# Kernel optimization log

Hardware: AMD Instinct MI355X
Metric: run time of the kernel (lower is better)

## Reference

```python
import jax, jax.numpy as jnp
import numpy as np

D_MODEL = 256; N_HEADS = 8; N_LEVELS = 4; N_POINTS = 4; D_FFN = 1024
BS = 8; NQ = 100; NKPT = 17
LEVEL_SHAPES = [(160, 160), (80, 80), (40, 40), (20, 20)]  # (H, W) per level
LEN_V = sum(h * w for h, w in LEVEL_SHAPES)  # 34000


def layer_norm(x, g, b, eps=1e-5):
    m = x.mean(-1, keepdims=True)
    v = ((x - m) ** 2).mean(-1, keepdims=True)
    return (x - m) * jax.lax.rsqrt(v + eps) * g + b


def mha(q, k, v, Wqkv, bqkv, Wo, bo):
    # torch nn.MultiheadAttention, batch_first, eval mode (no dropout)
    d = q.shape[-1]; dh = d // N_HEADS
    def proj(x, W, b):
        return (x @ W.T + b).reshape(*x.shape[:-1], N_HEADS, dh)
    qp = proj(q, Wqkv[:d], bqkv[:d])
    kp = proj(k, Wqkv[d:2 * d], bqkv[d:2 * d])
    vp = proj(v, Wqkv[2 * d:], bqkv[2 * d:])
    att = jnp.einsum('bqhd,bkhd->bhqk', qp, kp) / jnp.sqrt(jnp.asarray(dh, q.dtype))
    att = jax.nn.softmax(att, -1)
    out = jnp.einsum('bhqk,bkhd->bqhd', att, vp).reshape(q.shape)
    return out @ Wo.T + bo


def bilinear_sample(val, loc, h, w):
    # val: (B, H, h*w, Dh); loc: (B, Lq, H, P, 2) normalized to [0,1]
    # matches F.grid_sample(align_corners=False, padding_mode='zeros') on grid 2*loc-1
    B, Lq, H, P, _ = loc.shape
    px = loc[..., 0] * w - 0.5
    py = loc[..., 1] * h - 0.5
    x0f = jnp.floor(px); y0f = jnp.floor(py)
    lx = px - x0f; ly = py - y0f
    x0 = x0f.astype(jnp.int32); y0 = y0f.astype(jnp.int32)
    out = jnp.zeros((B, H, Lq, P, val.shape[-1]), val.dtype)
    for dx, dy, wt in ((0, 0, (1 - lx) * (1 - ly)), (1, 0, lx * (1 - ly)),
                       (0, 1, (1 - lx) * ly), (1, 1, lx * ly)):
        xi = x0 + dx; yi = y0 + dy
        valid = ((xi >= 0) & (xi < w) & (yi >= 0) & (yi < h)).astype(val.dtype)
        idx = jnp.clip(yi, 0, h - 1) * w + jnp.clip(xi, 0, w - 1)  # (B,Lq,H,P)
        idx = idx.transpose(0, 2, 1, 3).reshape(B, H, Lq * P)
        g = jnp.take_along_axis(val, idx[..., None], axis=2).reshape(B, H, Lq, P, -1)
        out = out + g * (wt * valid).transpose(0, 2, 1, 3)[..., None]
    return out  # (B, H, Lq, P, Dh)


def ms_deform_attn(query, ref_points, memory, off_W, off_b, aw_W, aw_b,
                   val_W, val_b, outp_W, outp_b):
    B, Lq, _ = query.shape
    dh = D_MODEL // N_HEADS
    value = (memory @ val_W.T + val_b).reshape(B, LEN_V, N_HEADS, dh)
    off = (query @ off_W.T + off_b).reshape(B, Lq, N_HEADS, N_LEVELS, N_POINTS, 2)
    aw = (query @ aw_W.T + aw_b).reshape(B, Lq, N_HEADS, N_LEVELS * N_POINTS)
    aw = jax.nn.softmax(aw, -1).reshape(B, Lq, N_HEADS, N_LEVELS, N_POINTS)
    normalizer = jnp.array([[w, h] for h, w in LEVEL_SHAPES], dtype=query.dtype)  # (L,2) as (W,H)
    loc = ref_points[:, :, None, :, None, :] + off / normalizer[None, None, None, :, None, :]
    out = jnp.zeros((B, Lq, N_HEADS, dh), query.dtype)
    start = 0
    for l, (h, w) in enumerate(LEVEL_SHAPES):
        vl = value[:, start:start + h * w].transpose(0, 2, 1, 3)  # (B,H,hw,Dh)
        s = bilinear_sample(vl, loc[:, :, :, l], h, w)            # (B,H,Lq,P,Dh)
        out = out + jnp.einsum('bhqpd,bqhp->bqhd', s, aw[:, :, :, l])
        start += h * w
    return out.reshape(B, Lq, D_MODEL) @ outp_W.T + outp_b


def setup_inputs() -> dict:
    key = jax.random.key(0)
    ks = iter(jax.random.split(key, 40))
    d = D_MODEL
    def w(shape, s=0.02):
        return jax.random.normal(next(ks), shape, jnp.float32) * s
    inp = {
        'tgt_pose': jax.random.normal(next(ks), (BS, NQ, NKPT, d), jnp.float32),
        'tgt_pose_query_pos': jax.random.normal(next(ks), (BS, NQ, NKPT, d), jnp.float32),
        'tgt_pose_reference_points': jax.random.uniform(next(ks), (BS, NQ * NKPT, N_LEVELS, 2), jnp.float32),
        'memory': jax.random.normal(next(ks), (BS, LEN_V, d), jnp.float32),
        'win_Wqkv': w((3 * d, d)), 'win_bqkv': jnp.zeros((3 * d,), jnp.float32),
        'win_Wo': w((d, d)), 'win_bo': jnp.zeros((d,), jnp.float32),
        'win_ng': jnp.ones((d,), jnp.float32), 'win_nb': jnp.zeros((d,), jnp.float32),
        'acr_Wqkv': w((3 * d, d)), 'acr_bqkv': jnp.zeros((3 * d,), jnp.float32),
        'acr_Wo': w((d, d)), 'acr_bo': jnp.zeros((d,), jnp.float32),
        'acr_ng': jnp.ones((d,), jnp.float32), 'acr_nb': jnp.zeros((d,), jnp.float32),
        'off_W': w((N_HEADS * N_LEVELS * N_POINTS * 2, d)),
        'off_b': jax.random.uniform(next(ks), (N_HEADS * N_LEVELS * N_POINTS * 2,), jnp.float32, -1.0, 1.0),
        'aw_W': w((N_HEADS * N_LEVELS * N_POINTS, d)), 'aw_b': jnp.zeros((N_HEADS * N_LEVELS * N_POINTS,), jnp.float32),
        'val_W': w((d, d)), 'val_b': jnp.zeros((d,), jnp.float32),
        'outp_W': w((d, d)), 'outp_b': jnp.zeros((d,), jnp.float32),
        'gate_W': w((2 * d, 2 * d)), 'gate_b': jnp.zeros((2 * d,), jnp.float32),
        'gate_ng': jnp.ones((d,), jnp.float32), 'gate_nb': jnp.zeros((d,), jnp.float32),
        'ffn_W1': w((D_FFN, d)), 'ffn_b1': jnp.zeros((D_FFN,), jnp.float32),
        'ffn_W2': w((d, D_FFN)), 'ffn_b2': jnp.zeros((d,), jnp.float32),
        'n2_g': jnp.ones((d,), jnp.float32), 'n2_b': jnp.zeros((d,), jnp.float32),
        'memory_spatial_shapes': jnp.array(LEVEL_SHAPES, jnp.int32),
    }
    return inp


def reference(tgt_pose, tgt_pose_query_pos, tgt_pose_reference_points, memory,
              win_Wqkv, win_bqkv, win_Wo, win_bo, win_ng, win_nb,
              acr_Wqkv, acr_bqkv, acr_Wo, acr_bo, acr_ng, acr_nb,
              off_W, off_b, aw_W, aw_b, val_W, val_b, outp_W, outp_b,
              gate_W, gate_b, gate_ng, gate_nb,
              ffn_W1, ffn_b1, ffn_W2, ffn_b2, n2_g, n2_b,
              memory_spatial_shapes):
    bs, nq, K, d = tgt_pose.shape
    # with_pos_embed mutates tgt_pose in place in the torch code -> residual includes pos
    tgt = tgt_pose + tgt_pose_query_pos
    # within-attention over keypoints of each query
    x = tgt.reshape(bs * nq, K, d)
    t2 = mha(x, x, x, win_Wqkv, win_bqkv, win_Wo, win_bo).reshape(bs, nq, K, d)
    tgt = layer_norm(tgt + t2, win_ng, win_nb)
    # across-attention over queries for each keypoint
    xk = tgt.transpose(0, 2, 1, 3).reshape(bs * K, nq, d)
    t2 = mha(xk, xk, xk, acr_Wqkv, acr_bqkv, acr_Wo, acr_bo)
    tgt = layer_norm(xk + t2, acr_ng, acr_nb).reshape(bs, K, nq, d).transpose(0, 2, 1, 3)
    # second in-place pos add before deformable cross-attn (also feeds gateway)
    tgt_q = tgt + tgt_pose_query_pos
    t2 = ms_deform_attn(tgt_q.reshape(bs, nq * K, d), tgt_pose_reference_points, memory,
                        off_W, off_b, aw_W, aw_b, val_W, val_b, outp_W, outp_b)
    t2 = t2.reshape(bs, nq, K, d)
    # Gate
    g = jax.nn.sigmoid(jnp.concatenate([tgt_q, t2], -1) @ gate_W.T + gate_b)
    g1, g2 = jnp.split(g, 2, -1)
    tgt = layer_norm(g1 * tgt_q + g2 * t2, gate_ng, gate_nb)
    # FFN
    h = jax.nn.relu(tgt @ ffn_W1.T + ffn_b1)
    tgt = tgt + h @ ffn_W2.T + ffn_b2
    tgt = layer_norm(jnp.clip(tgt, -65504.0, 65504.0), n2_g, n2_b)
    return tgt
```

## Files before the change

kernel.cpp:

```cpp
#include <hip/hip_runtime.h>
#include <hip/hip_bf16.h>

#define NH 8
#define BS_ 8
#define NQ_ 100
#define NK_ 17
#define LQ 1700
#define T_TOK 13600
#define LEN_VV 34000

typedef __attribute__((ext_vector_type(8))) short short8v;
typedef __attribute__((ext_vector_type(8))) __bf16 bf16x8;
typedef __attribute__((ext_vector_type(4))) float f32x4;

__device__ __forceinline__ short f2bf(float f){
  __hip_bfloat16 h = __float2bfloat16(f);
  return *reinterpret_cast<short*>(&h);
}
__device__ __forceinline__ float bf2f(short s){
  return __uint_as_float(((uint)(unsigned short)s) << 16);
}

template<int EPI, int ADDA, int SWZ, int INB>
__global__ __launch_bounds__(256) void mgemm_k(const void* __restrict__ Av,
                                               const float* __restrict__ A2,
                                               const float* __restrict__ W,
                                               const float* __restrict__ bias,
                                               __hip_bfloat16* __restrict__ Cb,
                                               int M, int N, int K, int nbx){
  __shared__ short sh[128 * 136];
  short* As = sh;
  short* Ws = sh + 128 * 64;
  int j;
  if (SWZ){
    int total = gridDim.x;
    int q = total >> 3, r = total & 7;
    int x = blockIdx.x & 7, k = blockIdx.x >> 3;
    j = (x < r) ? x * (q + 1) + k : r * (q + 1) + (x - r) * q + k;
  } else {
    j = blockIdx.x;
  }
  const float* A = (const float*)Av;
  const short* Ab = (const short*)Av;
  const int tid = threadIdx.x;
  const int bm = (j / nbx) * 128, bn = (j % nbx) * 128;
  const int wave = tid >> 6, lane = tid & 63;
  const int wm = (wave >> 1) * 64, wn = (wave & 1) * 64;
  const int s = tid & 7;
  const int row0 = tid >> 3;
  f32x4 acc[4][4] = {};
  const int lrow = lane & 15, lk = lane >> 4;

  float4 ra[INB ? 1 : 8], rw[8];
  short8v rab[INB ? 4 : 1];
#pragma unroll
  for (int i = 0; i < 4; i++){
    int row = row0 + i * 32;
    int gr = bm + row;
    if (INB){
      short8v z = {};
      rab[INB ? i : 0] = (gr < M) ? *(const short8v*)(Ab + (size_t)gr * K + s * 8) : z;
    } else {
      float4 z = make_float4(0.f, 0.f, 0.f, 0.f);
      if (gr < M){
        const float* p = A + (size_t)gr * K + s * 8;
        float4 x0 = ((const float4*)p)[0], x1 = ((const float4*)p)[1];
        if (ADDA){
          const float* q2 = A2 + (size_t)gr * K + s * 8;
          float4 y0 = ((const float4*)q2)[0], y1 = ((const float4*)q2)[1];
          x0.x+=y0.x; x0.y+=y0.y; x0.z+=y0.z; x0.w+=y0.w;
          x1.x+=y1.x; x1.y+=y1.y; x1.z+=y1.z; x1.w+=y1.w;
        }
        ra[INB ? 0 : (2 * i)] = x0; ra[INB ? 0 : (2 * i + 1)] = x1;
      } else { ra[INB ? 0 : (2 * i)] = z; ra[INB ? 0 : (2 * i + 1)] = z; }
    }
    const float* q = W + (size_t)(bn + row) * K + s * 8;
    rw[2 * i] = ((const float4*)q)[0]; rw[2 * i + 1] = ((const float4*)q)[1];
  }

  for (int k0 = 0; k0 < K; k0 += 64){
#pragma unroll
    for (int i = 0; i < 4; i++){
      int row = row0 + i * 32;
      int sw = ((s ^ (row & 7)) << 3) + row * 64;
      if (INB){
        *(short8v*)&As[sw] = rab[INB ? i : 0];
      } else {
        float4 a0 = ra[INB ? 0 : (2 * i)], a1 = ra[INB ? 0 : (2 * i + 1)];
        short8v v;
        v[0]=f2bf(a0.x); v[1]=f2bf(a0.y); v[2]=f2bf(a0.z); v[3]=f2bf(a0.w);
        v[4]=f2bf(a1.x); v[5]=f2bf(a1.y); v[6]=f2bf(a1.z); v[7]=f2bf(a1.w);
        *(short8v*)&As[sw] = v;
      }
      float4 a0 = rw[2 * i], a1 = rw[2 * i + 1];
      short8v u;
      u[0]=f2bf(a0.x); u[1]=f2bf(a0.y); u[2]=f2bf(a0.z); u[3]=f2bf(a0.w);
      u[4]=f2bf(a1.x); u[5]=f2bf(a1.y); u[6]=f2bf(a1.z); u[7]=f2bf(a1.w);
      *(short8v*)&Ws[sw] = u;
    }
    __syncthreads();
    if (k0 + 64 < K){
#pragma unroll
      for (int i = 0; i < 4; i++){
        int row = row0 + i * 32;
        int gr = bm + row;
        if (INB){
          short8v z = {};
          rab[INB ? i : 0] = (gr < M) ? *(const short8v*)(Ab + (size_t)gr * K + k0 + 64 + s * 8) : z;
        } else {
          float4 z = make_float4(0.f, 0.f, 0.f, 0.f);
          if (gr < M){
            const float* p = A + (size_t)gr * K + k0 + 64 + s * 8;
            float4 x0 = ((const float4*)p)[0], x1 = ((const float4*)p)[1];
            if (ADDA){
              const float* q2 = A2 + (size_t)gr * K + k0 + 64 + s * 8;
              float4 y0 = ((const float4*)q2)[0], y1 = ((const float4*)q2)[1];
              x0.x+=y0.x; x0.y+=y0.y; x0.z+=y0.z; x0.w+=y0.w;
              x1.x+=y1.x; x1.y+=y1.y; x1.z+=y1.z; x1.w+=y1.w;
            }
            ra[INB ? 0 : (2 * i)] = x0; ra[INB ? 0 : (2 * i + 1)] = x1;
          } else { ra[INB ? 0 : (2 * i)] = z; ra[INB ? 0 : (2 * i + 1)] = z; }
        }
        const float* q = W + (size_t)(bn + row) * K + k0 + 64 + s * 8;
        rw[2 * i] = ((const float4*)q)[0]; rw[2 * i + 1] = ((const float4*)q)[1];
      }
    }
#pragma unroll
    for (int ks = 0; ks < 2; ks++){
      short8v af[4], bw[4];
      int slot = ks * 4 + lk;
#pragma unroll
      for (int m = 0; m < 4; m++){
        int r = wm + m * 16 + lrow;
        af[m] = *(const short8v*)&As[r * 64 + ((slot ^ (r & 7)) << 3)];
      }
#pragma unroll
      for (int n = 0; n < 4; n++){
        int r = wn + n * 16 + lrow;
        bw[n] = *(const short8v*)&Ws[r * 64 + ((slot ^ (r & 7)) << 3)];
      }
#pragma unroll
      for (int m = 0; m < 4; m++)
#pragma unroll
        for (int n = 0; n < 4; n++)
          acc[m][n] = __builtin_amdgcn_mfma_f32_16x16x32_bf16(
              __builtin_bit_cast(bf16x8, af[m]),
              __builtin_bit_cast(bf16x8, bw[n]), acc[m][n], 0, 0, 0);
    }
    __syncthreads();
  }
  const int STR = 136;
// ... 12 lines not shown
      }
    }
  }
  __syncthreads();
#pragma unroll
  for (int it = 0; it < 8; it++){
    int r = it * 16 + (tid >> 4);
    int chunk = tid & 15;
    if (bm + r < M){
      uint4 v = *(const uint4*)((const char*)sh + r * 272 + chunk * 16);
      *(uint4*)((char*)Cb + ((size_t)(bm + r) * N + bn) * 2 + chunk * 16) = v;
    }
  }
}

template<int EPI, int OUTB, int INB, int DUALA>
__global__ __launch_bounds__(256) void g64_k(const void* __restrict__ Av,
                                             const void* __restrict__ A1v,
                                             const float* __restrict__ W0,
                                             const float* __restrict__ W1,
                                             int NSPLIT,
                                             const float* __restrict__ bias0,
                                             const float* __restrict__ bias1,
                                             const float* __restrict__ RES,
                                             float* __restrict__ Cf,
                                             __hip_bfloat16* __restrict__ Cb,
                                             int M, int N, int K, int sA){
  __shared__ short sh64[2 * 64 * 64];
  short* As = sh64;
  short* Ws = sh64 + 64 * 64;
  const int tid = threadIdx.x;
  const int bn = blockIdx.x * 64, bm = blockIdx.y * 64;
  const int wave = tid >> 6, lane = tid & 63;
  const int wm = (wave >> 1) * 32, wn = (wave & 1) * 32;
  const int s = tid & 7, row0 = tid >> 3;
  const int lrow = lane & 15, lk = lane >> 4;
  f32x4 acc[2][2] = {};

  for (int k0 = 0; k0 < K; k0 += 64){
#pragma unroll
    for (int i = 0; i < 2; i++){
      int row = row0 + i * 32;
      int sw = ((s ^ (row & 7)) << 3) + row * 64;
      short8v v = {};
      int gr = bm + row;
      if (gr < M){
        if (INB){
          v = *(const short8v*)((const short*)Av + (size_t)gr * sA + k0 + s * 8);
        } else {
          const float* Ap;
          if (DUALA) Ap = (k0 < 256) ? (const float*)Av + (size_t)gr * 256 + k0
                                     : (const float*)A1v + (size_t)gr * 256 + (k0 - 256);
          else Ap = (const float*)Av + (size_t)gr * sA + k0;
          float4 a0 = ((const float4*)(Ap + s * 8))[0];
          float4 a1 = ((const float4*)(Ap + s * 8))[1];
          v[0]=f2bf(a0.x); v[1]=f2bf(a0.y); v[2]=f2bf(a0.z); v[3]=f2bf(a0.w);
          v[4]=f2bf(a1.x); v[5]=f2bf(a1.y); v[6]=f2bf(a1.z); v[7]=f2bf(a1.w);
        }
      }
      *(short8v*)&As[sw] = v;
      int wr = bn + row;
      const float* Wp = (wr < NSPLIT) ? W0 + (size_t)wr * K + k0
                                      : W1 + (size_t)(wr - NSPLIT) * K + k0;
      float4 b0 = ((const float4*)(Wp + s * 8))[0];
      float4 b1 = ((const float4*)(Wp + s * 8))[1];
      short8v u;
      u[0]=f2bf(b0.x); u[1]=f2bf(b0.y); u[2]=f2bf(b0.z); u[3]=f2bf(b0.w);
      u[4]=f2bf(b1.x); u[5]=f2bf(b1.y); u[6]=f2bf(b1.z); u[7]=f2bf(b1.w);
      *(short8v*)&Ws[sw] = u;
    }
    __syncthreads();
#pragma unroll
    for (int ks = 0; ks < 2; ks++){
      int slot = ks * 4 + lk;
      short8v af[2], bw[2];
#pragma unroll
      for (int m = 0; m < 2; m++){
        int r = wm + m * 16 + lrow;
        af[m] = *(const short8v*)&As[r * 64 + ((slot ^ (r & 7)) << 3)];
      }
#pragma unroll
      for (int n = 0; n < 2; n++){
        int r = wn + n * 16 + lrow;
        bw[n] = *(const short8v*)&Ws[r * 64 + ((slot ^ (r & 7)) << 3)];
      }
#pragma unroll
      for (int m = 0; m < 2; m++)
#pragma unroll
        for (int n = 0; n < 2; n++)
          acc[m][n] = __builtin_amdgcn_mfma_f32_16x16x32_bf16(
              __builtin_bit_cast(bf16x8, af[m]),
              __builtin_bit_cast(bf16x8, bw[n]), acc[m][n], 0, 0, 0);
    }
    __syncthreads();
  }
  if (OUTB){
    const int STR = 72;
#pragma unroll
    for (int n = 0; n < 2; n++){
      int col = wn + n * 16 + lrow;
      int gc = bn + col;
      float bsv = (gc < NSPLIT) ? bias0[gc] : bias1[gc - NSPLIT];
#pragma unroll
      for (int m = 0; m < 2; m++){
#pragma unroll
        for (int i = 0; i < 4; i++){
          int row = wm + m * 16 + lk * 4 + i;
          float c = acc[m][n][i] + bsv;
          if (EPI == 1) c = fmaxf(c, 0.f);
          if (EPI == 2) c = 1.f / (1.f + expf(-c));
          sh64[row * STR + col] = f2bf(c);
        }
      }
    }
    __syncthreads();
#pragma unroll
    for (int it = 0; it < 2; it++){
      int r = it * 32 + (tid >> 3);
      int chunk = tid & 7;
      if (bm + r < M){
        uint4 v = *(const uint4*)((const char*)sh64 + r * 144 + chunk * 16);
        *(uint4*)((char*)Cb + ((size_t)(bm + r) * N + bn) * 2 + chunk * 16) = v;
      }
    }
  } else {
#pragma unroll
    for (int n = 0; n < 2; n++){
      int gc = bn + wn + n * 16 + lrow;
      float bsv = (gc < NSPLIT) ? bias0[gc] : bias1[gc - NSPLIT];
#pragma unroll
      for (int m = 0; m < 2; m++){
#pragma unroll
        for (int i = 0; i < 4; i++){
          int row = bm + wm + m * 16 + lk * 4 + i;
          if (row >= M) continue;
          float c = acc[m][n][i] + bsv;
          if (EPI == 1) c = fmaxf(c, 0.f);
          if (EPI == 2) c = 1.f / (1.f + expf(-c));
          if (EPI == 3) c += RES[(size_t)row * N + gc];
          Cf[(size_t)row * N + gc] = c;
        }
      }
    }
  }
}

template<int SITE, int OUTB>
__global__ __launch_bounds__(512) void gln_k(const short* __restrict__ Abf,
                                             const float* __restrict__ W,
                                             const float* __restrict__ bias,
                                             const float* __restrict__ r0,
                                             const float* __restrict__ r1,
                                             const float* __restrict__ g,
                                             const float* __restrict__ be,
                                             void* __restrict__ outv,
                                             int M, int K){
  __shared__ short As[64 * 64];
  __shared__ short Ws[256 * 64];
  __shared__ float part[64][4][2];
  __shared__ float stats[64][2];
  const int tid = threadIdx.x;
  const int bm = blockIdx.x * 64;
  const int wave = tid >> 6, lane = tid & 63;
  const int wm = (wave >> 2) * 32, wn = (wave & 3) * 64;
  const int s = tid & 7, row0 = tid >> 3;
  const int lrow = lane & 15, lk = lane >> 4;
  f32x4 acc[2][4] = {};

  short8v pa = {};
  { int gr = bm + row0; if (gr < M) pa = *(const short8v*)(Abf + (size_t)gr * K + s * 8); }
  float4 pw[8];
#pragma unroll
  for (int i = 0; i < 4; i++){
    const float* wp = W + (size_t)(row0 + i * 64) * K + s * 8;
    pw[2 * i] = ((const float4*)wp)[0]; pw[2 * i + 1] = ((const float4*)wp)[1];
  }

  for (int k0 = 0; k0 < K; k0 += 64){
    *(short8v*)&As[row0 * 64 + ((s ^ (row0 & 7)) << 3)] = pa;
#pragma unroll
    for (int i = 0; i < 4; i++){
      int row = row0 + i * 64;
      float4 b0 = pw[2 * i], b1 = pw[2 * i + 1];
      short8v u;
      u[0]=f2bf(b0.x); u[1]=f2bf(b0.y); u[2]=f2bf(b0.z); u[3]=f2bf(b0.w);
      u[4]=f2bf(b1.x); u[5]=f2bf(b1.y); u[6]=f2bf(b1.z); u[7]=f2bf(b1.w);
      *(short8v*)&Ws[row * 64 + ((s ^ (row & 7)) << 3)] = u;
    }
    __syncthreads();
    if (k0 + 64 < K){
      int gr = bm + row0;
      pa = (short8v){};
      if (gr < M) pa = *(const short8v*)(Abf + (size_t)gr * K + k0 + 64 + s * 8);
#pragma unroll
      for (int i = 0; i < 4; i++){
        const float* wp = W + (size_t)(row0 + i * 64) * K + k0 + 64 + s * 8;
        pw[2 * i] = ((const float4*)wp)[0]; pw[2 * i + 1] = ((const float4*)wp)[1];
      }
    }
#pragma unroll
    for (int ks = 0; ks < 2; ks++){
      int slot = ks * 4 + lk;
      short8v af[2], bw[4];
#pragma unroll
      for (int m = 0; m < 2; m++){
        int r = wm + m * 16 + lrow;
        af[m] = *(const short8v*)&As[r * 64 + ((slot ^ (r & 7)) << 3)];
      }
#pragma unroll
      for (int n = 0; n < 4; n++){
        int r = wn + n * 16 + lrow;
        bw[n] = *(const short8v*)&Ws[r * 64 + ((slot ^ (r & 7)) << 3)];
      }
#pragma unroll
      for (int m = 0; m < 2; m++)
#pragma unroll
        for (int n = 0; n < 4; n++)
          acc[m][n] = __builtin_amdgcn_mfma_f32_16x16x32_bf16(
              __builtin_bit_cast(bf16x8, af[m]),
              __builtin_bit_cast(bf16x8, bw[n]), acc[m][n], 0, 0, 0);
    }
    __syncthreads();
  }

#pragma unroll
  for (int m = 0; m < 2; m++){
#pragma unroll
    for (int i = 0; i < 4; i++){
      int row = wm + m * 16 + lk * 4 + i;
      int grow = bm + row;
      float s1 = 0.f, s2 = 0.f;
      if (grow < M){
#pragma unroll
        for (int n = 0; n < 4; n++){
          int col = wn + n * 16 + lrow;
          float x = acc[m][n][i] + bias[col] + r0[(size_t)grow * 256 + col];
          if (SITE == 0) x += r1[(size_t)grow * 256 + col];
          if (SITE == 2) x = fminf(fmaxf(x, -65504.f), 65504.f);
          acc[m][n][i] = x;
          s1 += x; s2 += x * x;
        }
      }
#pragma unroll
      for (int msk = 1; msk <= 8; msk <<= 1){
        s1 += __shfl_xor(s1, msk, 64);
        s2 += __shfl_xor(s2, msk, 64);
      }
      if (lrow == 0){ part[row][wave & 3][0] = s1; part[row][wave & 3][1] = s2; }
    }
  }
  __syncthreads();
  if (tid < 64){
    float s1 = part[tid][0][0] + part[tid][1][0] + part[tid][2][0] + part[tid][3][0];
    float s2 = part[tid][0][1] + part[tid][1][1] + part[tid][2][1] + part[tid][3][1];
    float mean = s1 * (1.f / 256.f);
    float var = s2 * (1.f / 256.f) - mean * mean;
    stats[tid][0] = mean;
    stats[tid][1] = rsqrtf(fmaxf(var, 0.f) + 1e-5f);
  }
  __syncthreads();
#pragma unroll
  for (int m = 0; m < 2; m++){
#pragma unroll
    for (int i = 0; i < 4; i++){
      int row = wm + m * 16 + lk * 4 + i;
      int grow = bm + row;
      if (grow >= M) continue;
      float mean = stats[row][0], rstd = stats[row][1];
      size_t orow = grow;
      if (SITE == 0){
        int bi = grow / LQ; int rem = grow % LQ; int q = rem / NK_; int kk = rem % NK_;
        orow = (size_t)bi * LQ + kk * NQ_ + q;
      }
#pragma unroll
      for (int n = 0; n < 4; n++){
        int col = wn + n * 16 + lrow;
        float o = (acc[m][n][i] - mean) * rstd * g[col] + be[col];
        if (OUTB) ((short*)outv)[orow * 256 + col] = f2bf(o);
        else      ((float*)outv)[orow * 256 + col] = o;
      }
    }
  }
}

__global__ __launch_bounds__(512) void glnoa_k(const short* __restrict__ Abf,
                                               const float* __restrict__ W,
                                               const float* __restrict__ bias,
                                               const short* __restrict__ r0b,
                                               const float* __restrict__ qpos,
                                               const float* __restrict__ g,
                                               const float* __restrict__ be,
                                               short* __restrict__ TQout,
                                               float* __restrict__ OFFAW,
                                               const float* __restrict__ off_W,
                                               const float* __restrict__ aw_W,
                                               const float* __restrict__ off_b,
                                               const float* __restrict__ aw_b,
                                               int M){
  __shared__ short smem[64 * 256 + 384 * 64];
  short* As1 = smem;
  short* Ws1 = smem + 64 * 64;
  float* part = (float*)(smem + 64 * 64 + 256 * 64);
  float* stats = part + 64 * 4 * 2;
  short* As2 = smem;
  short* Ws2 = smem + 64 * 256;
  const int K = 256;
  const int tid = threadIdx.x;
  const int bm = blockIdx.x * 64;
  const int wave = tid >> 6, lane = tid & 63;
  const int wm = (wave >> 2) * 32, wn = (wave & 3) * 64;
  const int s = tid & 7, row0 = tid >> 3;
  const int lrow = lane & 15, lk = lane >> 4;
  f32x4 acc[2][4] = {};

  short8v pa = {};
  { int gr = bm + row0; if (gr < M) pa = *(const short8v*)(Abf + (size_t)gr * K + s * 8); }
  float4 pw[8];
#pragma unroll
  for (int i = 0; i < 4; i++){
    const float* wp = W + (size_t)(row0 + i * 64) * K + s * 8;
    pw[2 * i] = ((const float4*)wp)[0]; pw[2 * i + 1] = ((const float4*)wp)[1];
  }
  for (int k0 = 0; k0 < K; k0 += 64){
    *(short8v*)&As1[row0 * 64 + ((s ^ (row0 & 7)) << 3)] = pa;
#pragma unroll
    for (int i = 0; i < 4; i++){
      int row = row0 + i * 64;
      float4 b0 = pw[2 * i], b1 = pw[2 * i + 1];
      short8v u;
      u[0]=f2bf(b0.x); u[1]=f2bf(b0.y); u[2]=f2bf(b0.z); u[3]=f2bf(b0.w);
      u[4]=f2bf(b1.x); u[5]=f2bf(b1.y); u[6]=f2bf(b1.z); u[7]=f2bf(b1.w);
      *(short8v*)&Ws1[row * 64 + ((s ^ (row & 7)) << 3)] = u;
    }
    __syncthreads();
    if (k0 + 64 < K){
      int gr = bm + row0;
      pa = (short8v){};
      if (gr < M) pa = *(const short8v*)(Abf + (size_t)gr * K + k0 + 64 + s * 8);
#pragma unroll
      for (int i = 0; i < 4; i++){
        const float* wp = W + (size_t)(row0 + i * 64) * K + k0 + 64 + s * 8;
        pw[2 * i] = ((const float4*)wp)[0]; pw[2 * i + 1] = ((const float4*)wp)[1];
      }
    }
#pragma unroll
    for (int ks = 0; ks < 2; ks++){
      int slot = ks * 4 + lk;
      short8v af[2], bw[4];
#pragma unroll
      for (int m = 0; m < 2; m++){
        int r = wm + m * 16 + lrow;
        af[m] = *(const short8v*)&As1[r * 64 + ((slot ^ (r & 7)) << 3)];
      }
#pragma unroll
      for (int n = 0; n < 4; n++){
        int r = wn + n * 16 + lrow;
        bw[n] = *(const short8v*)&Ws1[r * 64 + ((slot ^ (r & 7)) << 3)];
      }
#pragma unroll
      for (int m = 0; m < 2; m++)
#pragma unroll
        for (int n = 0; n < 4; n++)
          acc[m][n] = __builtin_amdgcn_mfma_f32_16x16x32_bf16(
              __builtin_bit_cast(bf16x8, af[m]),
              __builtin_bit_cast(bf16x8, bw[n]), acc[m][n], 0, 0, 0);
    }
    __syncthreads();
  }
#pragma unroll
  for (int m = 0; m < 2; m++){
#pragma unroll
    for (int i = 0; i < 4; i++){
      int row = wm + m * 16 + lk * 4 + i;
      int grow = bm + row;
      float s1 = 0.f, s2 = 0.f;
      if (grow < M){
#pragma unroll
        for (int n = 0; n < 4; n++){
          int col = wn + n * 16 + lrow;
          float x = acc[m][n][i] + bias[col] + bf2f(r0b[(size_t)grow * 256 + col]);
          acc[m][n][i] = x;
          s1 += x; s2 += x * x;
        }
      }
#pragma unroll
      for (int msk = 1; msk <= 8; msk <<= 1){
        s1 += __shfl_xor(s1, msk, 64);
        s2 += __shfl_xor(s2, msk, 64);
      }
      if (lrow == 0){ part[(row * 4 + (wave & 3)) * 2] = s1; part[(row * 4 + (wave & 3)) * 2 + 1] = s2; }
    }
  }
  __syncthreads();
  if (tid < 64){
    float s1 = part[(tid * 4 + 0) * 2] + part[(tid * 4 + 1) * 2] + part[(tid * 4 + 2) * 2] + part[(tid * 4 + 3) * 2];
    float s2 = part[(tid * 4 + 0) * 2 + 1] + part[(tid * 4 + 1) * 2 + 1] + part[(tid * 4 + 2) * 2 + 1] + part[(tid * 4 + 3) * 2 + 1];
    float mean = s1 * (1.f / 256.f);
    float var = s2 * (1.f / 256.f) - mean * mean;
    stats[tid * 2] = mean;
    stats[tid * 2 + 1] = rsqrtf(fmaxf(var, 0.f) + 1e-5f);
  }
  __syncthreads();
#pragma unroll
  for (int m = 0; m < 2; m++){
#pragma unroll
    for (int i = 0; i < 4; i++){
      int row = wm + m * 16 + lk * 4 + i;
      int grow = bm + row;
      float mean = stats[row * 2], rstd = stats[row * 2 + 1];
      size_t orow = 0;
      if (grow < M){
        int bi = grow / LQ; int rem = grow % LQ; int kk = rem / NQ_; int q = rem % NQ_;
        orow = (size_t)bi * LQ + q * NK_ + kk;
      }
#pragma unroll
      for (int n = 0; n < 4; n++){
        int col = wn + n * 16 + lrow;
        float tq = 0.f;
        if (grow < M){
          float o = (acc[m][n][i] - mean) * rstd * g[col] + be[col];
          tq = o + qpos[orow * 256 + col];
          TQout[orow * 256 + col] = f2bf(tq);
        }
        As2[row * 256 + ((((col >> 3) ^ (row & 7)) << 3) + (col & 7))] = f2bf(tq);
      }
    }
  }
  __syncthreads();
  const int wm2 = (wave >> 2) * 32, wn2 = (wave & 3) * 96;
  f32x4 acc2[2][6] = {};
  for (int k0 = 0; k0 < 256; k0 += 64){
#pragma unroll
    for (int it = 0; it < 6; it++){
      int wr = row0 + it * 64;
      const float* Wp = (wr < 256) ? off_W + (size_t)wr * 256 + k0
                                   : aw_W + (size_t)(wr - 256) * 256 + k0;
      float4 b0 = ((const float4*)(Wp + s * 8))[0];
      float4 b1 = ((const float4*)(Wp + s * 8))[1];
      short8v u;
      u[0]=f2bf(b0.x); u[1]=f2bf(b0.y); u[2]=f2bf(b0.z); u[3]=f2bf(b0.w);
      u[4]=f2bf(b1.x); u[5]=f2bf(b1.y); u[6]=f2bf(b1.z); u[7]=f2bf(b1.w);
      *(short8v*)&Ws2[wr * 64 + ((s ^ (wr & 7)) << 3)] = u;
    }
    __syncthreads();
#pragma unroll
    for (int ks = 0; ks < 2; ks++){
      int slotl = ks * 4 + lk;
      int slotg = (k0 >> 3) + slotl;
      short8v af[2], bw[6];
#pragma unroll
      for (int m = 0; m < 2; m++){
        int r = wm2 + m * 16 + lrow;
        af[m] = *(const short8v*)&As2[r * 256 + ((slotg ^ (r & 7)) << 3)];
      }
#pragma unroll
      for (int n = 0; n < 6; n++){
        int r = wn2 + n * 16 + lrow;
        bw[n] = *(const short8v*)&Ws2[r * 64 + ((slotl ^ (r & 7)) << 3)];
      }
#pragma unroll
      for (int m = 0; m < 2; m++)
#pragma unroll
        for (int n = 0; n < 6; n++)
          acc2[m][n] = __builtin_amdgcn_mfma_f32_16x16x32_bf16(
              __builtin_bit_cast(bf16x8, af[m]),
              __builtin_bit_cast(bf16x8, bw[n]), acc2[m][n], 0, 0, 0);
    }
    __syncthreads();
  }
#pragma unroll
  for (int m = 0; m < 2; m++){
#pragma unroll
    for (int i = 0; i < 4; i++){
      int row = wm2 + m * 16 + lk * 4 + i;
      int grow = bm + row;
      if (grow >= M) continue;
      int bi = grow / LQ; int rem = grow % LQ; int kk = rem / NQ_; int q = rem % NQ_;
      size_t orow = (size_t)bi * LQ + q * NK_ + kk;
#pragma unroll
      for (int n = 0; n < 6; n++){
        int col = wn2 + n * 16 + lrow;
        float c = acc2[m][n][i] + ((col < 256) ? off_b[col] : aw_b[col - 256]);
        OFFAW[orow * 384 + col] = c;
      }
    }
  }
}

__global__ __launch_bounds__(512) void gateln_k(const short* __restrict__ TQ,
                                                const short* __restrict__ T2,
                                                const float* __restrict__ W,
                                                const float* __restrict__ bias,
                                                const float* __restrict__ g,
                                                const float* __restrict__ be,
                                                float* __restrict__ out, int M){
  __shared__ short sh[64 * 64 + 512 * 64];
  short* As = sh;
  short* Ws = sh + 64 * 64;
  const int tid = threadIdx.x;
  const int bm = blockIdx.x * 64;
  const int wave = tid >> 6, lane = tid & 63;
  const int wm = (wave >> 2) * 32, wn = (wave & 3) * 128;
  const int s = tid & 7, row0 = tid >> 3;
  const int lrow = lane & 15, lk = lane >> 4;
  f32x4 acc[2][8] = {};

  for (int k0 = 0; k0 < 512; k0 += 64){
    {
      short8v v = {};
      int gr = bm + row0;
      if (gr < M){
        v = (k0 < 256) ? *(const short8v*)(TQ + (size_t)gr * 256 + k0 + s * 8)
                       : *(const short8v*)(T2 + (size_t)gr * 256 + (k0 - 256) + s * 8);
      }
      *(short8v*)&As[row0 * 64 + ((s ^ (row0 & 7)) << 3)] = v;
    }
#pragma unroll
    for (int i = 0; i < 8; i++){
      int row = row0 + i * 64;
      const float* wp = W + (size_t)row * 512 + k0 + s * 8;
      float4 b0 = ((const float4*)wp)[0], b1 = ((const float4*)wp)[1];
      short8v u;
      u[0]=f2bf(b0.x); u[1]=f2bf(b0.y); u[2]=f2bf(b0.z); u[3]=f2bf(b0.w);
      u[4]=f2bf(b1.x); u[5]=f2bf(b1.y); u[6]=f2bf(b1.z); u[7]=f2bf(b1.w);
      *(short8v*)&Ws[row * 64 + ((s ^ (row & 7)) << 3)] = u;
    }
    __syncthreads();
#pragma unroll
    for (int ks = 0; ks < 2; ks++){
      int slot = ks * 4 + lk;
      short8v af[2], bw[8];
#pragma unroll
      for (int m = 0; m < 2; m++){
        int r = wm + m * 16 + lrow;
        af[m] = *(const short8v*)&As[r * 64 + ((slot ^ (r & 7)) << 3)];
      }
#pragma unroll
      for (int n = 0; n < 8; n++){
        int r = wn + n * 16 + lrow;
        bw[n] = *(const short8v*)&Ws[r * 64 + ((slot ^ (r & 7)) << 3)];
      }
#pragma unroll
      for (int m = 0; m < 2; m++)
#pragma unroll
        for (int n = 0; n < 8; n++)
          acc[m][n] = __builtin_amdgcn_mfma_f32_16x16x32_bf16(
              __builtin_bit_cast(bf16x8, af[m]),
              __builtin_bit_cast(bf16x8, bw[n]), acc[m][n], 0, 0, 0);
    }
    __syncthreads();
  }
  short* gb = sh;
  const int GSTR = 520;
#pragma unroll
  for (int n = 0; n < 8; n++){
    int col = wn + n * 16 + lrow;
    float bsv = bias[col];
#pragma unroll
    for (int m = 0; m < 2; m++){
#pragma unroll
      for (int i = 0; i < 4; i++){
        int row = wm + m * 16 + lk * 4 + i;
        float c = acc[m][n][i] + bsv;
        gb[row * GSTR + col] = f2bf(1.f / (1.f + __expf(-c)));
      }
    }
  }
  __syncthreads();
  {
    int row = tid >> 3, cg = tid & 7;
    int grow = bm + row;
    float x[32];
    float s1 = 0.f, s2 = 0.f;
    if (grow < M){
#pragma unroll
      for (int jv = 0; jv < 4; jv++){
        int c0 = cg * 32 + jv * 8;
        short8v aqv = *(const short8v*)(TQ + (size_t)grow * 256 + c0);
        short8v t2v = *(const short8v*)(T2 + (size_t)grow * 256 + c0);
#pragma unroll
        for (int jj = 0; jj < 8; jj++){
          float g1 = bf2f(gb[row * GSTR + c0 + jj]);
          float g2 = bf2f(gb[row * GSTR + 256 + c0 + jj]);
          float xv = g1 * bf2f(aqv[jj]) + g2 * bf2f(t2v[jj]);
          x[jv * 8 + jj] = xv; s1 += xv; s2 += xv * xv;
        }
      }
    }
    s1 += __shfl_xor(s1, 1, 64); s2 += __shfl_xor(s2, 1, 64);
    s1 += __shfl_xor(s1, 2, 64); s2 += __shfl_xor(s2, 2, 64);
    s1 += __shfl_xor(s1, 4, 64); s2 += __shfl_xor(s2, 4, 64);
    float mean = s1 * (1.f / 256.f);
    float var = s2 * (1.f / 256.f) - mean * mean;
    float rstd = rsqrtf(fmaxf(var, 0.f) + 1e-5f);
    if (grow < M){
#pragma unroll
      for (int jv = 0; jv < 4; jv++){
        int c0 = cg * 32 + jv * 8;
        float4 o0, o1;
#pragma unroll
        for (int jj = 0; jj < 8; jj++){
          int c = c0 + jj;
          float o = (x[jv * 8 + jj] - mean) * rstd * g[c] + be[c];
          if (jj < 4) ((float*)&o0)[jj] = o; else ((float*)&o1)[jj - 4] = o;
        }
        *(float4*)(out + (size_t)grow * 256 + c0) = o0;
        *(float4*)(out + (size_t)grow * 256 + c0 + 4) = o1;
      }
    }
  }
}

template<int TP, int NSPL>
__global__ __launch_bounds__(256) void mha_mfma_k(const short* __restrict__ qkv,
                                                  __hip_bfloat16* __restrict__ out, int S){
// ... 221 lines not shown
                              hipStream_t stream){
  const float* tgt_pose = (const float*)d_in[0];
  const float* qpos     = (const float*)d_in[1];
  const float* refp     = (const float*)d_in[2];
  const float* memory   = (const float*)d_in[3];
  const float* win_Wqkv = (const float*)d_in[4];
  const float* win_bqkv = (const float*)d_in[5];
  const float* win_Wo   = (const float*)d_in[6];
  const float* win_bo   = (const float*)d_in[7];
  const float* win_ng   = (const float*)d_in[8];
  const float* win_nb   = (const float*)d_in[9];
  const float* acr_Wqkv = (const float*)d_in[10];
  const float* acr_bqkv = (const float*)d_in[11];
  const float* acr_Wo   = (const float*)d_in[12];
  const float* acr_bo   = (const float*)d_in[13];
  const float* acr_ng   = (const float*)d_in[14];
  const float* acr_nb   = (const float*)d_in[15];
  const float* off_W    = (const float*)d_in[16];
  const float* off_b    = (const float*)d_in[17];
  const float* aw_W     = (const float*)d_in[18];
  const float* aw_b     = (const float*)d_in[19];
  const float* val_W    = (const float*)d_in[20];
  const float* val_b    = (const float*)d_in[21];
  const float* outp_W   = (const float*)d_in[22];
  const float* outp_b   = (const float*)d_in[23];
  const float* gate_W   = (const float*)d_in[24];
  const float* gate_b   = (const float*)d_in[25];
  const float* gate_ng  = (const float*)d_in[26];
  const float* gate_nb  = (const float*)d_in[27];
  const float* ffn_W1   = (const float*)d_in[28];
  const float* ffn_b1   = (const float*)d_in[29];
  const float* ffn_W2   = (const float*)d_in[30];
  const float* ffn_b2   = (const float*)d_in[31];
  const float* n2_g     = (const float*)d_in[32];
  const float* n2_b     = (const float*)d_in[33];

  float* out = (float*)d_out;
  char* ws = (char*)d_ws;
  const size_t TB = (size_t)T_TOK * 256 * 4;
  float* B2 = (float*)(ws);
  char* p = ws + TB;
  short* B1b = (short*)p;  p += (size_t)T_TOK * 256 * 2;
  short* Qb  = (short*)p;  p += (size_t)T_TOK * 768 * 2;
  short* ABF = (short*)p;  p += (size_t)T_TOK * 256 * 2;
  short* TQb = (short*)p;  p += (size_t)T_TOK * 256 * 2;
  short* T2b = (short*)p;  p += (size_t)T_TOK * 256 * 2;
  float* OFFAW = (float*)p; p += (size_t)T_TOK * 384 * 4;
  char* Vregion = p;
  __hip_bfloat16* V = (__hip_bfloat16*)Vregion;
  short* FF = (short*)Vregion;

  const int GM128 = (T_TOK + 127) / 128;
  const int GM64  = (T_TOK + 63) / 64;
  const int BIG = 1 << 30;

  mgemm_k<0,0,1,0><<<2 * 2125, 256, 0, stream>>>(memory, nullptr, val_W, val_b, V, BS_ * LEN_VV, 256, 256, 2);
  mgemm_k<0,1,0,0><<<6 * GM128, 256, 0, stream>>>(tgt_pose, qpos, win_Wqkv, win_bqkv, (__hip_bfloat16*)Qb, T_TOK, 768, 256, 6);
  mha_mfma_k<32,1><<<800 * 4, 256, 0, stream>>>(Qb, (__hip_bfloat16*)ABF, 17);
  gln_k<0,1><<<GM64, 512, 0, stream>>>(ABF, win_Wo, win_bo, tgt_pose, qpos, win_ng, win_nb, B1b, T_TOK, 256);
  mgemm_k<0,0,0,1><<<6 * GM128, 256, 0, stream>>>(B1b, nullptr, acr_Wqkv, acr_bqkv, (__hip_bfloat16*)Qb, T_TOK, 768, 256, 6);
  mha_mfma_k<112,2><<<136 * 8, 256, 0, stream>>>(Qb, (__hip_bfloat16*)ABF, 100);
  glnoa_k<<<GM64, 512, 0, stream>>>(ABF, acr_Wo, acr_bo, B1b, qpos, acr_ng, acr_nb,
                                    TQb, OFFAW, off_W, aw_W, off_b, aw_b, T_TOK);
  deform_k<<<T_TOK / 4, 256, 0, stream>>>(V, OFFAW, refp, (unsigned int*)ABF);
  g64_k<0,1,1,0><<<dim3(4, GM64), 256, 0, stream>>>(ABF, nullptr, outp_W, outp_W, BIG, outp_b, outp_b, nullptr, nullptr, (__hip_bfloat16*)T2b, T_TOK, 256, 256, 256);
  gateln_k<<<GM64, 512, 0, stream>>>(TQb, T2b, gate_W, gate_b, gate_ng, gate_nb, B2, T_TOK);
  mgemm_k<1,0,0,0><<<8 * GM128, 256, 0, stream>>>(B2, nullptr, ffn_W1, ffn_b1, (__hip_bfloat16*)FF, T_TOK, 1024, 256, 8);
  gln_k<2,0><<<GM64, 512, 0, stream>>>(FF, ffn_W2, ffn_b2, B2, nullptr, n2_g, n2_b, out, T_TOK, 1024);
}
```

Baseline: 463.7 us.

## Shrink fused GEMM+LayerNorm kernels to 32-row tiles with 256 threads

The fused GEMM+LayerNorm kernels (gln_k, glnoa_k, gateln_k) now use 32-row M tiles and 256-thread blocks instead of 64 rows and 512 threads, which doubles the grid size. The weight prefetch registers in gln_k/glnoa_k are converted to bf16 at load time, and a cvt8 helper factors out the fp32-to-bf16 packing. The goal is better CU occupancy and load balance on the fused row-LN kernels, since a full row must be resident per block. The cost is that each block re-stages the whole weight matrix for half as many rows, which doubles the weight traffic per row.

```diff
diff --git a/kernel.cpp b/kernel.cpp
--- a/kernel.cpp
+++ b/kernel.cpp
@@ -19,6 +19,12 @@
 }
 __device__ __forceinline__ float bf2f(short s){
   return __uint_as_float(((uint)(unsigned short)s) << 16);
+}
+__device__ __forceinline__ short8v cvt8(float4 a, float4 b){
+  short8v u;
+  u[0]=f2bf(a.x); u[1]=f2bf(a.y); u[2]=f2bf(a.z); u[3]=f2bf(a.w);
+  u[4]=f2bf(b.x); u[5]=f2bf(b.y); u[6]=f2bf(b.z); u[7]=f2bf(b.w);
+  return u;
 }
 
 template<int EPI, int ADDA, int SWZ, int INB>
@@ -86,17 +92,9 @@
       if (INB){
         *(short8v*)&As[sw] = rab[INB ? i : 0];
       } else {
-        float4 a0 = ra[INB ? 0 : (2 * i)], a1 = ra[INB ? 0 : (2 * i + 1)];
-        short8v v;
-        v[0]=f2bf(a0.x); v[1]=f2bf(a0.y); v[2]=f2bf(a0.z); v[3]=f2bf(a0.w);
-        v[4]=f2bf(a1.x); v[5]=f2bf(a1.y); v[6]=f2bf(a1.z); v[7]=f2bf(a1.w);
-        *(short8v*)&As[sw] = v;
-      }
-      float4 a0 = rw[2 * i], a1 = rw[2 * i + 1];
-      short8v u;
-      u[0]=f2bf(a0.x); u[1]=f2bf(a0.y); u[2]=f2bf(a0.z); u[3]=f2bf(a0.w);
-      u[4]=f2bf(a1.x); u[5]=f2bf(a1.y); u[6]=f2bf(a1.z); u[7]=f2bf(a1.w);
-      *(short8v*)&Ws[sw] = u;
+        *(short8v*)&As[sw] = cvt8(ra[INB ? 0 : (2 * i)], ra[INB ? 0 : (2 * i + 1)]);
+      }
+      *(short8v*)&Ws[sw] = cvt8(rw[2 * i], rw[2 * i + 1]);
     }
     __syncthreads();
     if (k0 + 64 < K){
@@ -215,22 +213,14 @@
           if (DUALA) Ap = (k0 < 256) ? (const float*)Av + (size_t)gr * 256 + k0
                                      : (const float*)A1v + (size_t)gr * 256 + (k0 - 256);
           else Ap = (const float*)Av + (size_t)gr * sA + k0;
-          float4 a0 = ((const float4*)(Ap + s * 8))[0];
-          float4 a1 = ((const float4*)(Ap + s * 8))[1];
-          v[0]=f2bf(a0.x); v[1]=f2bf(a0.y); v[2]=f2bf(a0.z); v[3]=f2bf(a0.w);
-          v[4]=f2bf(a1.x); v[5]=f2bf(a1.y); v[6]=f2bf(a1.z); v[7]=f2bf(a1.w);
+          v = cvt8(((const float4*)(Ap + s * 8))[0], ((const float4*)(Ap + s * 8))[1]);
         }
       }
       *(short8v*)&As[sw] = v;
       int wr = bn + row;
       const float* Wp = (wr < NSPLIT) ? W0 + (size_t)wr * K + k0
                                       : W1 + (size_t)(wr - NSPLIT) * K + k0;
-      float4 b0 = ((const float4*)(Wp + s * 8))[0];
-      float4 b1 = ((const float4*)(Wp + s * 8))[1];
-      short8v u;
-      u[0]=f2bf(b0.x); u[1]=f2bf(b0.y); u[2]=f2bf(b0.z); u[3]=f2bf(b0.w);
-      u[4]=f2bf(b1.x); u[5]=f2bf(b1.y); u[6]=f2bf(b1.z); u[7]=f2bf(b1.w);
-      *(short8v*)&Ws[sw] = u;
+      *(short8v*)&Ws[sw] = cvt8(((const float4*)(Wp + s * 8))[0], ((const float4*)(Wp + s * 8))[1]);
     }
     __syncthreads();
 #pragma unroll
@@ -309,7 +299,7 @@
 }
 
 template<int SITE, int OUTB>
-__global__ __launch_bounds__(512) void gln_k(const short* __restrict__ Abf,
+__global__ __launch_bounds__(256) void gln_k(const short* __restrict__ Abf,
                                              const float* __restrict__ W,
                                              const float* __restrict__ bias,
                                              const float* __restrict__ r0,
@@ -318,37 +308,33 @@
                                              const float* __restrict__ be,
                                              void* __restrict__ outv,
                                              int M, int K){
-  __shared__ short As[64 * 64];
+  __shared__ short As[32 * 64];
   __shared__ short Ws[256 * 64];
-  __shared__ float part[64][4][2];
-  __shared__ float stats[64][2];
+  __shared__ float part[32][4][2];
+  __shared__ float stats[32][2];
   const int tid = threadIdx.x;
-  const int bm = blockIdx.x * 64;
+  const int bm = blockIdx.x * 32;
   const int wave = tid >> 6, lane = tid & 63;
-  const int wm = (wave >> 2) * 32, wn = (wave & 3) * 64;
+  const int wn = wave * 64;
   const int s = tid & 7, row0 = tid >> 3;
   const int lrow = lane & 15, lk = lane >> 4;
   f32x4 acc[2][4] = {};
 
   short8v pa = {};
   { int gr = bm + row0; if (gr < M) pa = *(const short8v*)(Abf + (size_t)gr * K + s * 8); }
-  float4 pw[8];
-#pragma unroll
-  for (int i = 0; i < 4; i++){
-    const float* wp = W + (size_t)(row0 + i * 64) * K + s * 8;
-    pw[2 * i] = ((const float4*)wp)[0]; pw[2 * i + 1] = ((const float4*)wp)[1];
+  short8v pwb[8];
+#pragma unroll
+  for (int i = 0; i < 8; i++){
+    const float* wp = W + (size_t)(row0 + i * 32) * K + s * 8;
+    pwb[i] = cvt8(((const float4*)wp)[0], ((const float4*)wp)[1]);
   }
 
   for (int k0 = 0; k0 < K; k0 += 64){
     *(short8v*)&As[row0 * 64 + ((s ^ (row0 & 7)) << 3)] = pa;
 #pragma unroll
-    for (int i = 0; i < 4; i++){
-      int row = row0 + i * 64;
-      float4 b0 = pw[2 * i], b1 = pw[2 * i + 1];
-      short8v u;
-      u[0]=f2bf(b0.x); u[1]=f2bf(b0.y); u[2]=f2bf(b0.z); u[3]=f2bf(b0.w);
-      u[4]=f2bf(b1.x); u[5]=f2bf(b1.y); u[6]=f2bf(b1.z); u[7]=f2bf(b1.w);
-      *(short8v*)&Ws[row * 64 + ((s ^ (row & 7)) << 3)] = u;
+    for (int i = 0; i < 8; i++){
+      int row = row0 + i * 32;
+      *(short8v*)&Ws[row * 64 + ((s ^ (row & 7)) << 3)] = pwb[i];
     }
     __syncthreads();
     if (k0 + 64 < K){
@@ -356,9 +342,9 @@
       pa = (short8v){};
       if (gr < M) pa = *(const short8v*)(Abf + (size_t)gr * K + k0 + 64 + s * 8);
 #pragma unroll
-      for (int i = 0; i < 4; i++){
-        const float* wp = W + (size_t)(row0 + i * 64) * K + k0 + 64 + s * 8;
-        pw[2 * i] = ((const float4*)wp)[0]; pw[2 * i + 1] = ((const float4*)wp)[1];
+      for (int i = 0; i < 8; i++){
+        const float* wp = W + (size_t)(row0 + i * 32) * K + k0 + 64 + s * 8;
+        pwb[i] = cvt8(((const float4*)wp)[0], ((const float4*)wp)[1]);
       }
     }
 #pragma unroll
@@ -367,7 +353,7 @@
       short8v af[2], bw[4];
 #pragma unroll
       for (int m = 0; m < 2; m++){
-        int r = wm + m * 16 + lrow;
+        int r = m * 16 + lrow;
         af[m] = *(const short8v*)&As[r * 64 + ((slot ^ (r & 7)) << 3)];
       }
 #pragma unroll
@@ -390,7 +376,7 @@
   for (int m = 0; m < 2; m++){
 #pragma unroll
     for (int i = 0; i < 4; i++){
-      int row = wm + m * 16 + lk * 4 + i;
+      int row = m * 16 + lk * 4 + i;
       int grow = bm + row;
       float s1 = 0.f, s2 = 0.f;
       if (grow < M){
@@ -409,11 +395,11 @@
         s1 += __shfl_xor(s1, msk, 64);
         s2 += __shfl_xor(s2, msk, 64);
       }
-      if (lrow == 0){ part[row][wave & 3][0] = s1; part[row][wave & 3][1] = s2; }
+      if (lrow == 0){ part[row][wave][0] = s1; part[row][wave][1] = s2; }
     }
   }
   __syncthreads();
-  if (tid < 64){
+  if (tid < 32){
     float s1 = part[tid][0][0] + part[tid][1][0] + part[tid][2][0] + part[tid][3][0];
     float s2 = part[tid][0][1] + part[tid][1][1] + part[tid][2][1] + part[tid][3][1];
     float mean = s1 * (1.f / 256.f);
@@ -426,7 +412,7 @@
   for (int m = 0; m < 2; m++){
 #pragma unroll
     for (int i = 0; i < 4; i++){
-      int row = wm + m * 16 + lk * 4 + i;
+      int row = m * 16 + lk * 4 + i;
       int grow = bm + row;
       if (grow >= M) continue;
       float mean = stats[row][0], rstd = stats[row][1];
@@ -446,7 +432,7 @@
   }
 }
 
-__global__ __launch_bounds__(512) void glnoa_k(const short* __restrict__ Abf,
+__global__ __launch_bounds__(256) void glnoa_k(const short* __restrict__ Abf,
                                                const float* __restrict__ W,
                                                const float* __restrict__ bias,
                                                const short* __restrict__ r0b,
@@ -460,40 +446,36 @@
                                                const float* __restrict__ off_b,
                                                const float* __restrict__ aw_b,
                                                int M){
-  __shared__ short smem[64 * 256 + 384 * 64];
+  __shared__ short smem[32 * 256 + 384 * 64];
+  __shared__ float part[32][4][2];
+  __shared__ float stats[32][2];
   short* As1 = smem;
-  short* Ws1 = smem + 64 * 64;
-  float* part = (float*)(smem + 64 * 64 + 256 * 64);
-  float* stats = part + 64 * 4 * 2;
+  short* Ws1 = smem + 32 * 64;
   short* As2 = smem;
-  short* Ws2 = smem + 64 * 256;
+  short* Ws2 = smem + 32 * 256;
   const int K = 256;
   const int tid = threadIdx.x;
-  const int bm = blockIdx.x * 64;
+  const int bm = blockIdx.x * 32;
   const int wave = tid >> 6, lane = tid & 63;
-  const int wm = (wave >> 2) * 32, wn = (wave & 3) * 64;
+  const int wn = wave * 64;
   const int s = tid & 7, row0 = tid >> 3;
   const int lrow = lane & 15, lk = lane >> 4;
   f32x4 acc[2][4] = {};
 
   short8v pa = {};
   { int gr = bm + row0; if (gr < M) pa = *(const short8v*)(Abf + (size_t)gr * K + s * 8); }
-  float4 pw[8];
-#pragma unroll
-  for (int i = 0; i < 4; i++){
-    const float* wp = W + (size_t)(row0 + i * 64) * K + s * 8;
-    pw[2 * i] = ((const float4*)wp)[0]; pw[2 * i + 1] = ((const float4*)wp)[1];
+  short8v pwb[8];
+#pragma unroll
+  for (int i = 0; i < 8; i++){
+    const float* wp = W + (size_t)(row0 + i * 32) * K + s * 8;
+    pwb[i] = cvt8(((const float4*)wp)[0], ((const float4*)wp)[1]);
   }
   for (int k0 = 0; k0 < K; k0 += 64){
     *(short8v*)&As1[row0 * 64 + ((s ^ (row0 & 7)) << 3)] = pa;
 #pragma unroll
-    for (int i = 0; i < 4; i++){
-      int row = row0 + i * 64;
-      float4 b0 = pw[2 * i], b1 = pw[2 * i + 1];
-      short8v u;
-      u[0]=f2bf(b0.x); u[1]=f2bf(b0.y); u[2]=f2bf(b0.z); u[3]=f2bf(b0.w);
-      u[4]=f2bf(b1.x); u[5]=f2bf(b1.y); u[6]=f2bf(b1.z); u[7]=f2bf(b1.w);
-      *(short8v*)&Ws1[row * 64 + ((s ^ (row & 7)) << 3)] = u;
+    for (int i = 0; i < 8; i++){
+      int row = row0 + i * 32;
+      *(short8v*)&Ws1[row * 64 + ((s ^ (row & 7)) << 3)] = pwb[i];
     }
     __syncthreads();
     if (k0 + 64 < K){
@@ -501,9 +483,9 @@
       pa = (short8v){};
       if (gr < M) pa = *(const short8v*)(Abf + (size_t)gr * K + k0 + 64 + s * 8);
 #pragma unroll
-      for (int i = 0; i < 4; i++){
-        const float* wp = W + (size_t)(row0 + i * 64) * K + k0 + 64 + s * 8;
-        pw[2 * i] = ((const float4*)wp)[0]; pw[2 * i + 1] = ((const float4*)wp)[1];
+      for (int i = 0; i < 8; i++){
+        const float* wp = W + (size_t)(row0 + i * 32) * K + k0 + 64 + s * 8;
+        pwb[i] = cvt8(((const float4*)wp)[0], ((const float4*)wp)[1]);
       }
     }
 #pragma unroll
@@ -512,7 +494,7 @@
       short8v af[2], bw[4];
 #pragma unroll
       for (int m = 0; m < 2; m++){
-        int r = wm + m * 16 + lrow;
+        int r = m * 16 + lrow;
         af[m] = *(const short8v*)&As1[r * 64 + ((slot ^ (r & 7)) << 3)];
       }
 #pragma unroll
@@ -534,7 +516,7 @@
   for (int m = 0; m < 2; m++){
 #pragma unroll
     for (int i = 0; i < 4; i++){
-      int row = wm + m * 16 + lk * 4 + i;
+      int row = m * 16 + lk * 4 + i;
       int grow = bm + row;
       float s1 = 0.f, s2 = 0.f;
       if (grow < M){
@@ -551,26 +533,26 @@
         s1 += __shfl_xor(s1, msk, 64);
         s2 += __shfl_xor(s2, msk, 64);
       }
-      if (lrow == 0){ part[(row * 4 + (wave & 3)) * 2] = s1; part[(row * 4 + (wave & 3)) * 2 + 1] = s2; }
+      if (lrow == 0){ part[row][wave][0] = s1; part[row][wave][1] = s2; }
     }
   }
   __syncthreads();
-  if (tid < 64){
-    float s1 = part[(tid * 4 + 0) * 2] + part[(tid * 4 + 1) * 2] + part[(tid * 4 + 2) * 2] + part[(tid * 4 + 3) * 2];
-    float s2 = part[(tid * 4 + 0) * 2 + 1] + part[(tid * 4 + 1) * 2 + 1] + part[(tid * 4 + 2) * 2 + 1] + part[(tid * 4 + 3) * 2 + 1];
+  if (tid < 32){
+    float s1 = part[tid][0][0] + part[tid][1][0] + part[tid][2][0] + part[tid][3][0];
+    float s2 = part[tid][0][1] + part[tid][1][1] + part[tid][2][1] + part[tid][3][1];
     float mean = s1 * (1.f / 256.f);
     float var = s2 * (1.f / 256.f) - mean * mean;
-    stats[tid * 2] = mean;
-    stats[tid * 2 + 1] = rsqrtf(fmaxf(var, 0.f) + 1e-5f);
+    stats[tid][0] = mean;
+    stats[tid][1] = rsqrtf(fmaxf(var, 0.f) + 1e-5f);
   }
   __syncthreads();
 #pragma unroll
   for (int m = 0; m < 2; m++){
 #pragma unroll
     for (int i = 0; i < 4; i++){
-      int row = wm + m * 16 + lk * 4 + i;
+      int row = m * 16 + lk * 4 + i;
       int grow = bm + row;
-      float mean = stats[row * 2], rstd = stats[row * 2 + 1];
+      float mean = stats[row][0], rstd = stats[row][1];
       size_t orow = 0;
       if (grow < M){
         int bi = grow / LQ; int rem = grow % LQ; int kk = rem / NQ_; int q = rem % NQ_;
@@ -590,20 +572,16 @@
     }
   }
   __syncthreads();
-  const int wm2 = (wave >> 2) * 32, wn2 = (wave & 3) * 96;
+  const int wn2 = wave * 96;
   f32x4 acc2[2][6] = {};
   for (int k0 = 0; k0 < 256; k0 += 64){
 #pragma unroll
-    for (int it = 0; it < 6; it++){
-      int wr = row0 + it * 64;
+    for (int it = 0; it < 12; it++){
+      int wr = row0 + it * 32;
       const float* Wp = (wr < 256) ? off_W + (size_t)wr * 256 + k0
                                    : aw_W + (size_t)(wr - 256) * 256 + k0;
-      float4 b0 = ((const float4*)(Wp + s * 8))[0];
-      float4 b1 = ((const float4*)(Wp + s * 8))[1];
-      short8v u;
-      u[0]=f2bf(b0.x); u[1]=f2bf(b0.y); u[2]=f2bf(b0.z); u[3]=f2bf(b0.w);
-      u[4]=f2bf(b1.x); u[5]=f2bf(b1.y); u[6]=f2bf(b1.z); u[7]=f2bf(b1.w);
-      *(short8v*)&Ws2[wr * 64 + ((s ^ (wr & 7)) << 3)] = u;
+      *(short8v*)&Ws2[wr * 64 + ((s ^ (wr & 7)) << 3)] =
+          cvt8(((const float4*)(Wp + s * 8))[0], ((const float4*)(Wp + s * 8))[1]);
     }
     __syncthreads();
 #pragma unroll
@@ -613,7 +591,7 @@
       short8v af[2], bw[6];
 #pragma unroll
       for (int m = 0; m < 2; m++){
-        int r = wm2 + m * 16 + lrow;
+        int r = m * 16 + lrow;
         af[m] = *(const short8v*)&As2[r * 256 + ((slotg ^ (r & 7)) << 3)];
       }
 #pragma unroll
@@ -635,7 +613,7 @@
   for (int m = 0; m < 2; m++){
 #pragma unroll
     for (int i = 0; i < 4; i++){
-      int row = wm2 + m * 16 + lk * 4 + i;
+      int row = m * 16 + lk * 4 + i;
       int grow = bm + row;
       if (grow >= M) continue;
       int bi = grow / LQ; int rem = grow % LQ; int kk = rem / NQ_; int q = rem % NQ_;
@@ -650,20 +628,20 @@
   }
 }
 
-__global__ __launch_bounds__(512) void gateln_k(const short* __restrict__ TQ,
+__global__ __launch_bounds__(256) void gateln_k(const short* __restrict__ TQ,
                                                 const short* __restrict__ T2,
                                                 const float* __restrict__ W,
                                                 const float* __restrict__ bias,
                                                 const float* __restrict__ g,
                                                 const float* __restrict__ be,
                                                 float* __restrict__ out, int M){
-  __shared__ short sh[64 * 64 + 512 * 64];
+  __shared__ short sh[32 * 64 + 512 * 64];
   short* As = sh;
-  short* Ws = sh + 64 * 64;
+  short* Ws = sh + 32 * 64;
   const int tid = threadIdx.x;
-  const int bm = blockIdx.x * 64;
+  const int bm = blockIdx.x * 32;
   const int wave = tid >> 6, lane = tid & 63;
-  const int wm = (wave >> 2) * 32, wn = (wave & 3) * 128;
+  const int wn = wave * 128;
   const int s = tid & 7, row0 = tid >> 3;
   const int lrow = lane & 15, lk = lane >> 4;
   f32x4 acc[2][8] = {};
@@ -679,14 +657,11 @@
       *(short8v*)&As[row0 * 64 + ((s ^ (row0 & 7)) << 3)] = v;
     }
 #pragma unroll
-    for (int i = 0; i < 8; i++){
-      int row = row0 + i * 64;
+    for (int i = 0; i < 16; i++){
+      int row = row0 + i * 32;
       const float* wp = W + (size_t)row * 512 + k0 + s * 8;
-      float4 b0 = ((const float4*)wp)[0], b1 = ((const float4*)wp)[1];
-      short8v u;
-      u[0]=f2bf(b0.x); u[1]=f2bf(b0.y); u[2]=f2bf(b0.z); u[3]=f2bf(b0.w);
-      u[4]=f2bf(b1.x); u[5]=f2bf(b1.y); u[6]=f2bf(b1.z); u[7]=f2bf(b1.w);
-      *(short8v*)&Ws[row * 64 + ((s ^ (row & 7)) << 3)] = u;
+      *(short8v*)&Ws[row * 64 + ((s ^ (row & 7)) << 3)] =
+          cvt8(((const float4*)wp)[0], ((const float4*)wp)[1]);
     }
     __syncthreads();
 #pragma unroll
@@ -695,7 +670,7 @@
       short8v af[2], bw[8];
 #pragma unroll
       for (int m = 0; m < 2; m++){
-        int r = wm + m * 16 + lrow;
+        int r = m * 16 + lrow;
         af[m] = *(const short8v*)&As[r * 64 + ((slot ^ (r & 7)) << 3)];
       }
 #pragma unroll
@@ -723,7 +698,7 @@
     for (int m = 0; m < 2; m++){
 #pragma unroll
       for (int i = 0; i < 4; i++){
-        int row = wm + m * 16 + lk * 4 + i;
+        int row = m * 16 + lk * 4 + i;
         float c = acc[m][n][i] + bsv;
         gb[row * GSTR + col] = f2bf(1.f / (1.f + __expf(-c)));
       }
@@ -1051,19 +1026,20 @@
 
   const int GM128 = (T_TOK + 127) / 128;
   const int GM64  = (T_TOK + 63) / 64;
+  const int GM32  = (T_TOK + 31) / 32;
   const int BIG = 1 << 30;
 
   mgemm_k<0,0,1,0><<<2 * 2125, 256, 0, stream>>>(memory, nullptr, val_W, val_b, V, BS_ * LEN_VV, 256, 256, 2);
   mgemm_k<0,1,0,0><<<6 * GM128, 256, 0, stream>>>(tgt_pose, qpos, win_Wqkv, win_bqkv, (__hip_bfloat16*)Qb, T_TOK, 768, 256, 6);
   mha_mfma_k<32,1><<<800 * 4, 256, 0, stream>>>(Qb, (__hip_bfloat16*)ABF, 17);
-  gln_k<0,1><<<GM64, 512, 0, stream>>>(ABF, win_Wo, win_bo, tgt_pose, qpos, win_ng, win_nb, B1b, T_TOK, 256);
+  gln_k<0,1><<<GM32, 256, 0, stream>>>(ABF, win_Wo, win_bo, tgt_pose, qpos, win_ng, win_nb, B1b, T_TOK, 256);
   mgemm_k<0,0,0,1><<<6 * GM128, 256, 0, stream>>>(B1b, nullptr, acr_Wqkv, acr_bqkv, (__hip_bfloat16*)Qb, T_TOK, 768, 256, 6);
   mha_mfma_k<112,2><<<136 * 8, 256, 0, stream>>>(Qb, (__hip_bfloat16*)ABF, 100);
-  glnoa_k<<<GM64, 512, 0, stream>>>(ABF, acr_Wo, acr_bo, B1b, qpos, acr_ng, acr_nb,
+  glnoa_k<<<GM32, 256, 0, stream>>>(ABF, acr_Wo, acr_bo, B1b, qpos, acr_ng, acr_nb,
                                     TQb, OFFAW, off_W, aw_W, off_b, aw_b, T_TOK);
   deform_k<<<T_TOK / 4, 256, 0, stream>>>(V, OFFAW, refp, (unsigned int*)ABF);
   g64_k<0,1,1,0><<<dim3(4, GM64), 256, 0, stream>>>(ABF, nullptr, outp_W, outp_W, BIG, outp_b, outp_b, nullptr, nullptr, (__hip_bfloat16*)T2b, T_TOK, 256, 256, 256);
-  gateln_k<<<GM64, 512, 0, stream>>>(TQb, T2b, gate_W, gate_b, gate_ng, gate_nb, B2, T_TOK);
+  gateln_k<<<GM32, 256, 0, stream>>>(TQb, T2b, gate_W, gate_b, gate_ng, gate_nb, B2, T_TOK);
   mgemm_k<1,0,0,0><<<8 * GM128, 256, 0, stream>>>(B2, nullptr, ffn_W1, ffn_b1, (__hip_bfloat16*)FF, T_TOK, 1024, 256, 8);
-  gln_k<2,0><<<GM64, 512, 0, stream>>>(FF, ffn_W2, ffn_b2, B2, nullptr, n2_g, n2_b, out, T_TOK, 1024);
+  gln_k<2,0><<<GM32, 256, 0, stream>>>(FF, ffn_W2, ffn_b2, B2, nullptr, n2_g, n2_b, out, T_TOK, 1024);
 }
```

Result: no change. 460.1 us (-0.8%).
